# Performance work log

Hardware: AMD Instinct MI355X
Metric: run time of the kernel (lower is better)

The kernel has to match this reference:

```python
import jax, jax.numpy as jnp
import numpy as np

PATCH = 3
ALPHA = 0.5
EPS = 1e-12  # F.normalize default eps


def _unfold(x, p):
    # nn.Unfold(kernel_size=p, padding=p//2) then reshape(B, C, p*p, H*W)
    B, C, H, W = x.shape
    pad = p // 2
    xp = jnp.pad(x, ((0, 0), (0, 0), (pad, pad), (pad, pad)))
    # kernel positions row-major, matching torch unfold channel-major layout
    pats = jnp.stack([xp[:, :, i:i + H, j:j + W]
                      for i in range(p) for j in range(p)], axis=2)  # [B,C,K,H,W]
    return pats.reshape(B, C, p * p, H * W)


def setup_inputs() -> dict:
    key = jax.random.key(0)
    k1, k2 = jax.random.split(key)
    B, C, H, W = 4, 32, 256, 256
    fe_lv = jax.random.normal(k1, (B, C, H, W), dtype=jnp.float32)
    fused_features = jax.random.normal(k2, (B, C, H, W), dtype=jnp.float32)
    return {"fe_lv": fe_lv, "fused_features": fused_features}


def reference(fe_lv, fused_features):
    B, C, H, W = fe_lv.shape
    N = H * W
    patches = _unfold(fused_features, PATCH)          # [B,C,K,N]
    fe_flat = fe_lv.reshape(B, C, N)                  # [B,C,N]

    # cosine similarity over channel dim
    pn = patches / jnp.maximum(jnp.linalg.norm(patches, axis=1, keepdims=True), EPS)
    fn = fe_flat / jnp.maximum(jnp.linalg.norm(fe_flat, axis=1, keepdims=True), EPS)
    cosine_sim = jnp.einsum('bckn,bcn->bnk', pn, fn)  # [B,N,K]
    cosine_weights = jax.nn.softmax(cosine_sim, axis=-1)

    # euclidean distance over channel dim
    dist = jnp.sqrt(jnp.sum((patches - fe_flat[:, :, None, :]) ** 2, axis=1))  # [B,K,N]
    euclidean_weights = jax.nn.softmax(-dist.transpose(0, 2, 1), axis=-1)      # [B,N,K]

    weights = ALPHA * cosine_weights + (1.0 - ALPHA) * euclidean_weights
    refined = jnp.einsum('bnk,bckn->bcn', weights, patches)  # [B,C,N]
    return refined.reshape(B, C, H, W) + fe_lv
```

## Files before the change

### kernel.cpp

```cpp
#include <hip/hip_runtime.h>
#include <math.h>

#define B_ 4
#define C_ 32
#define H_ 256
#define W_ 256
#define HW_ (H_ * W_)
#define K_ 9
#define TX 32
#define TY 4
#define HX 34
#define HY 6
#define HCH (HX * HY)
#define NOCT 4
#define FUH8 (NOCT * HCH)
#define EPS_ 1e-12f

typedef _Float16 h2v __attribute__((ext_vector_type(2)));
typedef _Float16 h8v __attribute__((ext_vector_type(8)));

#if defined(__has_builtin)
#if __has_builtin(__builtin_amdgcn_fdot2)
#define HAVE_FDOT2 1
#endif
#if __has_builtin(__builtin_amdgcn_cvt_pkrtz)
#define HAVE_PKRTZ 1
#endif
#endif

static __device__ __forceinline__ h2v pk2(float a, float b) {
#if defined(HAVE_PKRTZ)
    return __builtin_bit_cast(h2v, __builtin_amdgcn_cvt_pkrtz(a, b));
#else
    h2v r = {(_Float16)a, (_Float16)b};
    return r;
#endif
}

static __device__ __forceinline__ float dot2(h2v a, h2v b, float c) {
#if defined(HAVE_FDOT2)
    return __builtin_amdgcn_fdot2(a, b, c, false);
#else
    return c + (float)a[0] * (float)b[0] + (float)a[1] * (float)b[1];
#endif
}

__global__ __launch_bounds__(256, 6) void asfr_kernel(const float* __restrict__ fe,
                                                      const float* __restrict__ fu,
                                                      float* __restrict__ out) {
    __shared__ h8v lds8[FUH8];
    const int t = threadIdx.x;
    const int bx = blockIdx.x & 7;
    const int by = (blockIdx.x >> 3) & 63;
    const int b  = blockIdx.x >> 9;
    const int w0 = bx * TX, h0 = by * TY;

    const int x = t & 31;
    const int half = (t >> 5) & 1;
    const int y = t >> 6;
    const int c0 = half << 4;
    const int pxoff = b * (C_ * HW_) + (h0 + y) * W_ + (w0 + x);

    float fv[16];
#pragma unroll
    for (int cc = 0; cc < 16; ++cc) fv[cc] = fe[pxoff + (c0 + cc) * HW_];

    const float* fub = fu + b * (C_ * HW_);
#pragma unroll
    for (int j = 0; j < 3; ++j) {
        int u = t + j * 256;
        int oct = u / HCH;
        int pos = u - oct * HCH;
        int r = pos / HX;
        int col = pos - r * HX;
        int hh = h0 - 1 + r;
        int ww = w0 - 1 + col;
        bool ok = ((unsigned)hh < (unsigned)H_) && ((unsigned)ww < (unsigned)W_);
        int hcl = hh < 0 ? 0 : (hh > H_ - 1 ? H_ - 1 : hh);
        int wcl = ww < 0 ? 0 : (ww > W_ - 1 ? W_ - 1 : ww);
        const float* gp = fub + (oct * 8) * HW_ + hcl * W_ + wcl;
        float v[8];
#pragma unroll
        for (int c = 0; c < 8; ++c) v[c] = gp[c * HW_];
        float m = ok ? 1.f : 0.f;
#pragma unroll
        for (int c = 0; c < 8; ++c) v[c] *= m;
        h8v hv;
#pragma unroll
        for (int c = 0; c < 4; ++c) {
            h2v p = pk2(v[2 * c], v[2 * c + 1]);
            hv[2 * c] = p[0];
            hv[2 * c + 1] = p[1];
        }
        lds8[u] = hv;
    }
    if (t < FUH8 - 768) {
        int u = t + 768;
        int oct = u / HCH;
        int pos = u - oct * HCH;
        int r = pos / HX;
        int col = pos - r * HX;
        int hh = h0 - 1 + r;
        int ww = w0 - 1 + col;
        bool ok = ((unsigned)hh < (unsigned)H_) && ((unsigned)ww < (unsigned)W_);
        int hcl = hh < 0 ? 0 : (hh > H_ - 1 ? H_ - 1 : hh);
        int wcl = ww < 0 ? 0 : (ww > W_ - 1 ? W_ - 1 : ww);
        const float* gp = fub + (oct * 8) * HW_ + hcl * W_ + wcl;
        float v[8];
#pragma unroll
        for (int c = 0; c < 8; ++c) v[c] = gp[c * HW_];
        float m = ok ? 1.f : 0.f;
#pragma unroll
        for (int c = 0; c < 8; ++c) v[c] *= m;
        h8v hv;
#pragma unroll
        for (int c = 0; c < 4; ++c) {
            h2v p = pk2(v[2 * c], v[2 * c + 1]);
            hv[2 * c] = p[0];
            hv[2 * c + 1] = p[1];
        }
        lds8[u] = hv;
    }

    h8v fe8[2];
#pragma unroll
    for (int j = 0; j < 2; ++j) {
#pragma unroll
        for (int c = 0; c < 4; ++c) {
            h2v p = pk2(fv[8 * j + 2 * c], fv[8 * j + 2 * c + 1]);
            fe8[j][2 * c] = p[0];
            fe8[j][2 * c + 1] = p[1];
        }
    }
    __syncthreads();

    const int hc = (y + 1) * HX + (x + 1);
    const int koff[K_] = {-HX - 1, -HX, -HX + 1, -1, 0, 1, HX - 1, HX, HX + 1};

    float dot[K_], psq[K_];
#pragma unroll
    for (int k = 0; k < K_; ++k) { dot[k] = 0.f; psq[k] = 0.f; }
    float fsq = 0.f;

#pragma unroll
    for (int j = 0; j < 2; ++j) {
        const int oct = 2 * half + j;
        h8v fq = fe8[j];
        h2v fA0 = __builtin_shufflevector(fq, fq, 0, 1);
        h2v fA1 = __builtin_shufflevector(fq, fq, 2, 3);
        h2v fA2 = __builtin_shufflevector(fq, fq, 4, 5);
        h2v fA3 = __builtin_shufflevector(fq, fq, 6, 7);
        fsq = dot2(fA0, fA0, fsq);
        fsq = dot2(fA1, fA1, fsq);
        fsq = dot2(fA2, fA2, fsq);
        fsq = dot2(fA3, fA3, fsq);
        const h8v* fubase = &lds8[oct * HCH + hc];
#pragma unroll
        for (int k = 0; k < K_; ++k) {
            h8v p8 = fubase[koff[k]];
            h2v p0 = __builtin_shufflevector(p8, p8, 0, 1);
            h2v p1 = __builtin_shufflevector(p8, p8, 2, 3);
            h2v p2 = __builtin_shufflevector(p8, p8, 4, 5);
            h2v p3 = __builtin_shufflevector(p8, p8, 6, 7);
            dot[k] = dot2(p0, fA0, dot[k]);
            dot[k] = dot2(p1, fA1, dot[k]);
            dot[k] = dot2(p2, fA2, dot[k]);
            dot[k] = dot2(p3, fA3, dot[k]);
            psq[k] = dot2(p0, p0, psq[k]);
            psq[k] = dot2(p1, p1, psq[k]);
            psq[k] = dot2(p2, p2, psq[k]);
            psq[k] = dot2(p3, p3, psq[k]);
        }
    }

#pragma unroll
    for (int k = 0; k < K_; ++k) {
        dot[k] += __shfl_xor(dot[k], 32);
        psq[k] += __shfl_xor(psq[k], 32);
    }
    fsq += __shfl_xor(fsq, 32);

    float nf = fmaxf(sqrtf(fsq), EPS_);
    float cosv[K_], negd[K_];
#pragma unroll
    for (int k = 0; k < K_; ++k) {
        float np = fmaxf(sqrtf(psq[k]), EPS_);
        cosv[k] = __fdividef(dot[k], np * nf);
        float dsq = fmaxf(psq[k] - 2.f * dot[k] + fsq, 0.f);
        negd[k] = -sqrtf(dsq);
    }

    float m1 = cosv[0], m2 = negd[0];
#pragma unroll
    for (int k = 1; k < K_; ++k) { m1 = fmaxf(m1, cosv[k]); m2 = fmaxf(m2, negd[k]); }
    float s1 = 0.f, s2 = 0.f, e1[K_], e2[K_];
#pragma unroll
    for (int k = 0; k < K_; ++k) {
        e1[k] = __expf(cosv[k] - m1);
        e2[k] = __expf(negd[k] - m2);
        s1 += e1[k]; s2 += e2[k];
    }
    float r1 = __fdividef(0.5f, s1), r2 = __fdividef(0.5f, s2);
    h2v w2[K_];
#pragma unroll
    for (int k = 0; k < K_; ++k) {
        float wk = fmaf(e1[k], r1, e2[k] * r2);
        _Float16 wh = (_Float16)wk;
        h2v tmp = {wh, wh};
        w2[k] = tmp;
    }

#pragma unroll
    for (int j = 0; j < 2; ++j) {
        const int oct = 2 * half + j;
        const h8v* fubase = &lds8[oct * HCH + hc];
        h2v a0 = {(_Float16)0, (_Float16)0};
        h2v a1 = a0, a2 = a0, a3 = a0;
#pragma unroll
        for (int k = 0; k < K_; ++k) {
            h8v p8 = fubase[koff[k]];
            a0 += w2[k] * __builtin_shufflevector(p8, p8, 0, 1);
            a1 += w2[k] * __builtin_shufflevector(p8, p8, 2, 3);
            a2 += w2[k] * __builtin_shufflevector(p8, p8, 4, 5);
            a3 += w2[k] * __builtin_shufflevector(p8, p8, 6, 7);
        }
        h8v fq = fe8[j];
        const int cg = oct * 8;
        out[pxoff + (cg + 0) * HW_] = (float)(fq[0] + a0[0]);
        out[pxoff + (cg + 1) * HW_] = (float)(fq[1] + a0[1]);
        out[pxoff + (cg + 2) * HW_] = (float)(fq[2] + a1[0]);
        out[pxoff + (cg + 3) * HW_] = (float)(fq[3] + a1[1]);
        out[pxoff + (cg + 4) * HW_] = (float)(fq[4] + a2[0]);
        out[pxoff + (cg + 5) * HW_] = (float)(fq[5] + a2[1]);
        out[pxoff + (cg + 6) * HW_] = (float)(fq[6] + a3[0]);
        out[pxoff + (cg + 7) * HW_] = (float)(fq[7] + a3[1]);
    }
}

extern "C" void kernel_launch(void* const* d_in, const int* in_sizes, int n_in,
                              void* d_out, int out_size, void* d_ws, size_t ws_size,
                              hipStream_t stream) {
    const float* fe = (const float*)d_in[0];
    const float* fu = (const float*)d_in[1];
    float* out = (float*)d_out;
    dim3 grid((W_ / TX) * (H_ / TY) * B_), block(256);
    hipLaunchKernelGGL(asfr_kernel, grid, block, 0, stream, fe, fu, out);
}
```

Before: 33.28 us.

## Process two batches per block with double-buffered LDS and prefetched second tile

Each block now handles the same spatial tile for two batch images, b0 and b0+2, and the grid is halved. The second batch's halo tile is loaded into registers while the first batch is computed, then written to a second LDS buffer, so global latency overlaps with compute. Halo address and mask computation is hoisted and shared by both batches, and the LDS layout is padded to 256 entries per octet so index math uses shifts. In exchange the kernel holds 32 extra prefetch registers and twice the LDS, which may reduce occupancy, and the grid has fewer blocks.

New measurement: 34.09 us. +2.4%, slower.

```diff
diff --git a/kernel.cpp b/kernel.cpp
--- a/kernel.cpp
+++ b/kernel.cpp
@@ -13,7 +13,6 @@
 #define HY 6
 #define HCH (HX * HY)
 #define NOCT 4
-#define FUH8 (NOCT * HCH)
 #define EPS_ 1e-12f
 
 typedef _Float16 h2v __attribute__((ext_vector_type(2)));
@@ -48,29 +47,29 @@
 __global__ __launch_bounds__(256, 6) void asfr_kernel(const float* __restrict__ fe,
                                                       const float* __restrict__ fu,
                                                       float* __restrict__ out) {
-    __shared__ h8v lds8[FUH8];
+    __shared__ h8v lds8[2][NOCT * 256];
     const int t = threadIdx.x;
     const int bx = blockIdx.x & 7;
     const int by = (blockIdx.x >> 3) & 63;
-    const int b  = blockIdx.x >> 9;
+    const int b0 = blockIdx.x >> 9;
     const int w0 = bx * TX, h0 = by * TY;
+    const int TILE2 = 2 * C_ * HW_;
 
     const int x = t & 31;
     const int half = (t >> 5) & 1;
     const int y = t >> 6;
     const int c0 = half << 4;
-    const int pxoff = b * (C_ * HW_) + (h0 + y) * W_ + (w0 + x);
-
-    float fv[16];
-#pragma unroll
-    for (int cc = 0; cc < 16; ++cc) fv[cc] = fe[pxoff + (c0 + cc) * HW_];
-
-    const float* fub = fu + b * (C_ * HW_);
-#pragma unroll
-    for (int j = 0; j < 3; ++j) {
+    const int pxoff0 = b0 * (C_ * HW_) + (h0 + y) * W_ + (w0 + x);
+
+    int goff[4];
+    float msk[4];
+    bool vld[4];
+#pragma unroll
+    for (int j = 0; j < 4; ++j) {
         int u = t + j * 256;
-        int oct = u / HCH;
-        int pos = u - oct * HCH;
+        int oct = u >> 8;
+        int pos = u & 255;
+        vld[j] = pos < HCH;
         int r = pos / HX;
         int col = pos - r * HX;
         int hh = h0 - 1 + r;
@@ -78,162 +77,275 @@
         bool ok = ((unsigned)hh < (unsigned)H_) && ((unsigned)ww < (unsigned)W_);
         int hcl = hh < 0 ? 0 : (hh > H_ - 1 ? H_ - 1 : hh);
         int wcl = ww < 0 ? 0 : (ww > W_ - 1 ? W_ - 1 : ww);
-        const float* gp = fub + (oct * 8) * HW_ + hcl * W_ + wcl;
-        float v[8];
-#pragma unroll
-        for (int c = 0; c < 8; ++c) v[c] = gp[c * HW_];
-        float m = ok ? 1.f : 0.f;
-#pragma unroll
-        for (int c = 0; c < 8; ++c) v[c] *= m;
-        h8v hv;
-#pragma unroll
-        for (int c = 0; c < 4; ++c) {
-            h2v p = pk2(v[2 * c], v[2 * c + 1]);
-            hv[2 * c] = p[0];
-            hv[2 * c + 1] = p[1];
-        }
-        lds8[u] = hv;
-    }
-    if (t < FUH8 - 768) {
-        int u = t + 768;
-        int oct = u / HCH;
-        int pos = u - oct * HCH;
-        int r = pos / HX;
-        int col = pos - r * HX;
-        int hh = h0 - 1 + r;
-        int ww = w0 - 1 + col;
-        bool ok = ((unsigned)hh < (unsigned)H_) && ((unsigned)ww < (unsigned)W_);
-        int hcl = hh < 0 ? 0 : (hh > H_ - 1 ? H_ - 1 : hh);
-        int wcl = ww < 0 ? 0 : (ww > W_ - 1 ? W_ - 1 : ww);
-        const float* gp = fub + (oct * 8) * HW_ + hcl * W_ + wcl;
-        float v[8];
-#pragma unroll
-        for (int c = 0; c < 8; ++c) v[c] = gp[c * HW_];
-        float m = ok ? 1.f : 0.f;
-#pragma unroll
-        for (int c = 0; c < 8; ++c) v[c] *= m;
-        h8v hv;
-#pragma unroll
-        for (int c = 0; c < 4; ++c) {
-            h2v p = pk2(v[2 * c], v[2 * c + 1]);
-            hv[2 * c] = p[0];
-            hv[2 * c + 1] = p[1];
-        }
-        lds8[u] = hv;
-    }
-
-    h8v fe8[2];
-#pragma unroll
-    for (int j = 0; j < 2; ++j) {
+        goff[j] = (oct * 8) * HW_ + hcl * W_ + wcl;
+        msk[j] = ok ? 1.f : 0.f;
+    }
+
+    const float* fub0 = fu + b0 * (C_ * HW_);
+
+    float fv[16];
+#pragma unroll
+    for (int cc = 0; cc < 16; ++cc) fv[cc] = fe[pxoff0 + (c0 + cc) * HW_];
+
+#pragma unroll
+    for (int j = 0; j < 4; ++j) {
+        if (vld[j]) {
+            float v[8];
+#pragma unroll
+            for (int c = 0; c < 8; ++c) v[c] = fub0[goff[j] + c * HW_] * msk[j];
+            h8v hv;
+#pragma unroll
+            for (int c = 0; c < 4; ++c) {
+                h2v p = pk2(v[2 * c], v[2 * c + 1]);
+                hv[2 * c] = p[0];
+                hv[2 * c + 1] = p[1];
+            }
+            lds8[0][t + j * 256] = hv;
+        }
+    }
+    h8v fe80[2];
+#pragma unroll
+    for (int j = 0; j < 2; ++j)
 #pragma unroll
         for (int c = 0; c < 4; ++c) {
             h2v p = pk2(fv[8 * j + 2 * c], fv[8 * j + 2 * c + 1]);
-            fe8[j][2 * c] = p[0];
-            fe8[j][2 * c + 1] = p[1];
-        }
-    }
+            fe80[j][2 * c] = p[0];
+            fe80[j][2 * c + 1] = p[1];
+        }
     __syncthreads();
+
+    float s1[32];
+#pragma unroll
+    for (int j = 0; j < 4; ++j) {
+        if (vld[j]) {
+#pragma unroll
+            for (int c = 0; c < 8; ++c) s1[8 * j + c] = fub0[TILE2 + goff[j] + c * HW_];
+        }
+    }
 
     const int hc = (y + 1) * HX + (x + 1);
     const int koff[K_] = {-HX - 1, -HX, -HX + 1, -1, 0, 1, HX - 1, HX, HX + 1};
 
-    float dot[K_], psq[K_];
-#pragma unroll
-    for (int k = 0; k < K_; ++k) { dot[k] = 0.f; psq[k] = 0.f; }
-    float fsq = 0.f;
-
-#pragma unroll
-    for (int j = 0; j < 2; ++j) {
-        const int oct = 2 * half + j;
-        h8v fq = fe8[j];
-        h2v fA0 = __builtin_shufflevector(fq, fq, 0, 1);
-        h2v fA1 = __builtin_shufflevector(fq, fq, 2, 3);
-        h2v fA2 = __builtin_shufflevector(fq, fq, 4, 5);
-        h2v fA3 = __builtin_shufflevector(fq, fq, 6, 7);
-        fsq = dot2(fA0, fA0, fsq);
-        fsq = dot2(fA1, fA1, fsq);
-        fsq = dot2(fA2, fA2, fsq);
-        fsq = dot2(fA3, fA3, fsq);
-        const h8v* fubase = &lds8[oct * HCH + hc];
-#pragma unroll
-        for (int k = 0; k < K_; ++k) {
-            h8v p8 = fubase[koff[k]];
-            h2v p0 = __builtin_shufflevector(p8, p8, 0, 1);
-            h2v p1 = __builtin_shufflevector(p8, p8, 2, 3);
-            h2v p2 = __builtin_shufflevector(p8, p8, 4, 5);
-            h2v p3 = __builtin_shufflevector(p8, p8, 6, 7);
-            dot[k] = dot2(p0, fA0, dot[k]);
-            dot[k] = dot2(p1, fA1, dot[k]);
-            dot[k] = dot2(p2, fA2, dot[k]);
-            dot[k] = dot2(p3, fA3, dot[k]);
-            psq[k] = dot2(p0, p0, psq[k]);
-            psq[k] = dot2(p1, p1, psq[k]);
-            psq[k] = dot2(p2, p2, psq[k]);
-            psq[k] = dot2(p3, p3, psq[k]);
-        }
-    }
-
-#pragma unroll
-    for (int k = 0; k < K_; ++k) {
-        dot[k] += __shfl_xor(dot[k], 32);
-        psq[k] += __shfl_xor(psq[k], 32);
-    }
-    fsq += __shfl_xor(fsq, 32);
-
-    float nf = fmaxf(sqrtf(fsq), EPS_);
-    float cosv[K_], negd[K_];
-#pragma unroll
-    for (int k = 0; k < K_; ++k) {
-        float np = fmaxf(sqrtf(psq[k]), EPS_);
-        cosv[k] = __fdividef(dot[k], np * nf);
-        float dsq = fmaxf(psq[k] - 2.f * dot[k] + fsq, 0.f);
-        negd[k] = -sqrtf(dsq);
-    }
-
-    float m1 = cosv[0], m2 = negd[0];
-#pragma unroll
-    for (int k = 1; k < K_; ++k) { m1 = fmaxf(m1, cosv[k]); m2 = fmaxf(m2, negd[k]); }
-    float s1 = 0.f, s2 = 0.f, e1[K_], e2[K_];
-#pragma unroll
-    for (int k = 0; k < K_; ++k) {
-        e1[k] = __expf(cosv[k] - m1);
-        e2[k] = __expf(negd[k] - m2);
-        s1 += e1[k]; s2 += e2[k];
-    }
-    float r1 = __fdividef(0.5f, s1), r2 = __fdividef(0.5f, s2);
-    h2v w2[K_];
-#pragma unroll
-    for (int k = 0; k < K_; ++k) {
-        float wk = fmaf(e1[k], r1, e2[k] * r2);
-        _Float16 wh = (_Float16)wk;
-        h2v tmp = {wh, wh};
-        w2[k] = tmp;
-    }
-
-#pragma unroll
-    for (int j = 0; j < 2; ++j) {
-        const int oct = 2 * half + j;
-        const h8v* fubase = &lds8[oct * HCH + hc];
-        h2v a0 = {(_Float16)0, (_Float16)0};
-        h2v a1 = a0, a2 = a0, a3 = a0;
-#pragma unroll
-        for (int k = 0; k < K_; ++k) {
-            h8v p8 = fubase[koff[k]];
-            a0 += w2[k] * __builtin_shufflevector(p8, p8, 0, 1);
-            a1 += w2[k] * __builtin_shufflevector(p8, p8, 2, 3);
-            a2 += w2[k] * __builtin_shufflevector(p8, p8, 4, 5);
-            a3 += w2[k] * __builtin_shufflevector(p8, p8, 6, 7);
-        }
-        h8v fq = fe8[j];
-        const int cg = oct * 8;
-        out[pxoff + (cg + 0) * HW_] = (float)(fq[0] + a0[0]);
-        out[pxoff + (cg + 1) * HW_] = (float)(fq[1] + a0[1]);
-        out[pxoff + (cg + 2) * HW_] = (float)(fq[2] + a1[0]);
-        out[pxoff + (cg + 3) * HW_] = (float)(fq[3] + a1[1]);
-        out[pxoff + (cg + 4) * HW_] = (float)(fq[4] + a2[0]);
-        out[pxoff + (cg + 5) * HW_] = (float)(fq[5] + a2[1]);
-        out[pxoff + (cg + 6) * HW_] = (float)(fq[6] + a3[0]);
-        out[pxoff + (cg + 7) * HW_] = (float)(fq[7] + a3[1]);
+    {
+        float dot[K_], psq[K_];
+#pragma unroll
+        for (int k = 0; k < K_; ++k) { dot[k] = 0.f; psq[k] = 0.f; }
+        float fsq = 0.f;
+#pragma unroll
+        for (int j = 0; j < 2; ++j) {
+            const int oct = 2 * half + j;
+            h8v fq = fe80[j];
+            h2v fA0 = __builtin_shufflevector(fq, fq, 0, 1);
+            h2v fA1 = __builtin_shufflevector(fq, fq, 2, 3);
+            h2v fA2 = __builtin_shufflevector(fq, fq, 4, 5);
+            h2v fA3 = __builtin_shufflevector(fq, fq, 6, 7);
+            fsq = dot2(fA0, fA0, fsq);
+            fsq = dot2(fA1, fA1, fsq);
+            fsq = dot2(fA2, fA2, fsq);
+            fsq = dot2(fA3, fA3, fsq);
+            const h8v* fubase = &lds8[0][(oct << 8) + hc];
+#pragma unroll
+            for (int k = 0; k < K_; ++k) {
+                h8v p8 = fubase[koff[k]];
+                h2v p0 = __builtin_shufflevector(p8, p8, 0, 1);
+                h2v p1 = __builtin_shufflevector(p8, p8, 2, 3);
+                h2v p2 = __builtin_shufflevector(p8, p8, 4, 5);
+                h2v p3 = __builtin_shufflevector(p8, p8, 6, 7);
+                dot[k] = dot2(p0, fA0, dot[k]);
+                dot[k] = dot2(p1, fA1, dot[k]);
+                dot[k] = dot2(p2, fA2, dot[k]);
+                dot[k] = dot2(p3, fA3, dot[k]);
+                psq[k] = dot2(p0, p0, psq[k]);
+                psq[k] = dot2(p1, p1, psq[k]);
+                psq[k] = dot2(p2, p2, psq[k]);
+                psq[k] = dot2(p3, p3, psq[k]);
+            }
+        }
+#pragma unroll
+        for (int k = 0; k < K_; ++k) {
+            dot[k] += __shfl_xor(dot[k], 32);
+            psq[k] += __shfl_xor(psq[k], 32);
+        }
+        fsq += __shfl_xor(fsq, 32);
+
+        float nf = fmaxf(sqrtf(fsq), EPS_);
+        float cosv[K_], negd[K_];
+#pragma unroll
+        for (int k = 0; k < K_; ++k) {
+            float np = fmaxf(sqrtf(psq[k]), EPS_);
+            cosv[k] = __fdividef(dot[k], np * nf);
+            float dsq = fmaxf(psq[k] - 2.f * dot[k] + fsq, 0.f);
+            negd[k] = -sqrtf(dsq);
+        }
+        float m1 = cosv[0], m2 = negd[0];
+#pragma unroll
+        for (int k = 1; k < K_; ++k) { m1 = fmaxf(m1, cosv[k]); m2 = fmaxf(m2, negd[k]); }
+        float s1x = 0.f, s2x = 0.f, e1[K_], e2[K_];
+#pragma unroll
+        for (int k = 0; k < K_; ++k) {
+            e1[k] = __expf(cosv[k] - m1);
+            e2[k] = __expf(negd[k] - m2);
+            s1x += e1[k]; s2x += e2[k];
+        }
+        float r1 = __fdividef(0.5f, s1x), r2 = __fdividef(0.5f, s2x);
+        h2v w2[K_];
+#pragma unroll
+        for (int k = 0; k < K_; ++k) {
+            float wk = fmaf(e1[k], r1, e2[k] * r2);
+            _Float16 wh = (_Float16)wk;
+            h2v tmp = {wh, wh};
+            w2[k] = tmp;
+        }
+#pragma unroll
+        for (int j = 0; j < 2; ++j) {
+            const int oct = 2 * half + j;
+            const h8v* fubase = &lds8[0][(oct << 8) + hc];
+            h2v a0 = {(_Float16)0, (_Float16)0};
+            h2v a1 = a0, a2 = a0, a3 = a0;
+#pragma unroll
+            for (int k = 0; k < K_; ++k) {
+                h8v p8 = fubase[koff[k]];
+                a0 += w2[k] * __builtin_shufflevector(p8, p8, 0, 1);
+                a1 += w2[k] * __builtin_shufflevector(p8, p8, 2, 3);
+                a2 += w2[k] * __builtin_shufflevector(p8, p8, 4, 5);
+                a3 += w2[k] * __builtin_shufflevector(p8, p8, 6, 7);
+            }
+            h8v fq = fe80[j];
+            const int cg = oct * 8;
+            out[pxoff0 + (cg + 0) * HW_] = (float)(fq[0] + a0[0]);
+            out[pxoff0 + (cg + 1) * HW_] = (float)(fq[1] + a0[1]);
+            out[pxoff0 + (cg + 2) * HW_] = (float)(fq[2] + a1[0]);
+            out[pxoff0 + (cg + 3) * HW_] = (float)(fq[3] + a1[1]);
+            out[pxoff0 + (cg + 4) * HW_] = (float)(fq[4] + a2[0]);
+            out[pxoff0 + (cg + 5) * HW_] = (float)(fq[5] + a2[1]);
+            out[pxoff0 + (cg + 6) * HW_] = (float)(fq[6] + a3[0]);
+            out[pxoff0 + (cg + 7) * HW_] = (float)(fq[7] + a3[1]);
+        }
+    }
+
+#pragma unroll
+    for (int j = 0; j < 4; ++j) {
+        if (vld[j]) {
+            h8v hv;
+#pragma unroll
+            for (int c = 0; c < 4; ++c) {
+                h2v p = pk2(s1[8 * j + 2 * c] * msk[j], s1[8 * j + 2 * c + 1] * msk[j]);
+                hv[2 * c] = p[0];
+                hv[2 * c + 1] = p[1];
+            }
+            lds8[1][t + j * 256] = hv;
+        }
+    }
+    __syncthreads();
+
+    const int pxoff1 = pxoff0 + TILE2;
+    float fv1[16];
+#pragma unroll
+    for (int cc = 0; cc < 16; ++cc) fv1[cc] = fe[pxoff1 + (c0 + cc) * HW_];
+    h8v fe81[2];
+#pragma unroll
+    for (int j = 0; j < 2; ++j)
+#pragma unroll
+        for (int c = 0; c < 4; ++c) {
+            h2v p = pk2(fv1[8 * j + 2 * c], fv1[8 * j + 2 * c + 1]);
+            fe81[j][2 * c] = p[0];
+            fe81[j][2 * c + 1] = p[1];
+        }
+    {
+        float dot[K_], psq[K_];
+#pragma unroll
+        for (int k = 0; k < K_; ++k) { dot[k] = 0.f; psq[k] = 0.f; }
+        float fsq = 0.f;
+#pragma unroll
+        for (int j = 0; j < 2; ++j) {
+            const int oct = 2 * half + j;
+            h8v fq = fe81[j];
+            h2v fA0 = __builtin_shufflevector(fq, fq, 0, 1);
+            h2v fA1 = __builtin_shufflevector(fq, fq, 2, 3);
+            h2v fA2 = __builtin_shufflevector(fq, fq, 4, 5);
+            h2v fA3 = __builtin_shufflevector(fq, fq, 6, 7);
+            fsq = dot2(fA0, fA0, fsq);
+            fsq = dot2(fA1, fA1, fsq);
+            fsq = dot2(fA2, fA2, fsq);
+            fsq = dot2(fA3, fA3, fsq);
+            const h8v* fubase = &lds8[1][(oct << 8) + hc];
+#pragma unroll
+            for (int k = 0; k < K_; ++k) {
+                h8v p8 = fubase[koff[k]];
+                h2v p0 = __builtin_shufflevector(p8, p8, 0, 1);
+                h2v p1 = __builtin_shufflevector(p8, p8, 2, 3);
+                h2v p2 = __builtin_shufflevector(p8, p8, 4, 5);
+                h2v p3 = __builtin_shufflevector(p8, p8, 6, 7);
+                dot[k] = dot2(p0, fA0, dot[k]);
+                dot[k] = dot2(p1, fA1, dot[k]);
+                dot[k] = dot2(p2, fA2, dot[k]);
+                dot[k] = dot2(p3, fA3, dot[k]);
+                psq[k] = dot2(p0, p0, psq[k]);
+                psq[k] = dot2(p1, p1, psq[k]);
+                psq[k] = dot2(p2, p2, psq[k]);
+                psq[k] = dot2(p3, p3, psq[k]);
+            }
+        }
+#pragma unroll
+        for (int k = 0; k < K_; ++k) {
+            dot[k] += __shfl_xor(dot[k], 32);
+            psq[k] += __shfl_xor(psq[k], 32);
+        }
+        fsq += __shfl_xor(fsq, 32);
+
+        float nf = fmaxf(sqrtf(fsq), EPS_);
+        float cosv[K_], negd[K_];
+#pragma unroll
+        for (int k = 0; k < K_; ++k) {
+            float np = fmaxf(sqrtf(psq[k]), EPS_);
+            cosv[k] = __fdividef(dot[k], np * nf);
+            float dsq = fmaxf(psq[k] - 2.f * dot[k] + fsq, 0.f);
+            negd[k] = -sqrtf(dsq);
+        }
+        float m1 = cosv[0], m2 = negd[0];
+#pragma unroll
+        for (int k = 1; k < K_; ++k) { m1 = fmaxf(m1, cosv[k]); m2 = fmaxf(m2, negd[k]); }
+        float s1x = 0.f, s2x = 0.f, e1[K_], e2[K_];
+#pragma unroll
+        for (int k = 0; k < K_; ++k) {
+            e1[k] = __expf(cosv[k] - m1);
+            e2[k] = __expf(negd[k] - m2);
+            s1x += e1[k]; s2x += e2[k];
+        }
+        float r1 = __fdividef(0.5f, s1x), r2 = __fdividef(0.5f, s2x);
+        h2v w2[K_];
+#pragma unroll
+        for (int k = 0; k < K_; ++k) {
+            float wk = fmaf(e1[k], r1, e2[k] * r2);
+            _Float16 wh = (_Float16)wk;
+            h2v tmp = {wh, wh};
+            w2[k] = tmp;
+        }
+#pragma unroll
+        for (int j = 0; j < 2; ++j) {
+            const int oct = 2 * half + j;
+            const h8v* fubase = &lds8[1][(oct << 8) + hc];
+            h2v a0 = {(_Float16)0, (_Float16)0};
+            h2v a1 = a0, a2 = a0, a3 = a0;
+#pragma unroll
+            for (int k = 0; k < K_; ++k) {
+                h8v p8 = fubase[koff[k]];
+                a0 += w2[k] * __builtin_shufflevector(p8, p8, 0, 1);
+                a1 += w2[k] * __builtin_shufflevector(p8, p8, 2, 3);
+                a2 += w2[k] * __builtin_shufflevector(p8, p8, 4, 5);
+                a3 += w2[k] * __builtin_shufflevector(p8, p8, 6, 7);
+            }
+            h8v fq = fe81[j];
+            const int cg = oct * 8;
+            out[pxoff1 + (cg + 0) * HW_] = (float)(fq[0] + a0[0]);
+            out[pxoff1 + (cg + 1) * HW_] = (float)(fq[1] + a0[1]);
+            out[pxoff1 + (cg + 2) * HW_] = (float)(fq[2] + a1[0]);
+            out[pxoff1 + (cg + 3) * HW_] = (float)(fq[3] + a1[1]);
+            out[pxoff1 + (cg + 4) * HW_] = (float)(fq[4] + a2[0]);
+            out[pxoff1 + (cg + 5) * HW_] = (float)(fq[5] + a2[1]);
+            out[pxoff1 + (cg + 6) * HW_] = (float)(fq[6] + a3[0]);
+            out[pxoff1 + (cg + 7) * HW_] = (float)(fq[7] + a3[1]);
+        }
     }
 }
 
@@ -243,6 +355,6 @@
     const float* fe = (const float*)d_in[0];
     const float* fu = (const float*)d_in[1];
     float* out = (float*)d_out;
-    dim3 grid((W_ / TX) * (H_ / TY) * B_), block(256);
+    dim3 grid(8 * 64 * 2), block(256);
     hipLaunchKernelGGL(asfr_kernel, grid, block, 0, stream, fe, fu, out);
 }
```

## Reshape tile to 64x2 and batch all global loads before LDS staging

Applied to the files above, without the earlier changes.

Changes the spatial tile from 32x4 to 64x2 pixels per block, so the halo row width becomes 66 and each wavefront covers 32 contiguous columns with both channel halves. It also precomputes all gather offsets and masks, then issues every global load (fe and halo units) up front before packing to fp16 and writing LDS, raising memory-level parallelism. The halo grows from 816 to 1056 units per block, meaning more redundant loads and LDS (about 16.9 KB), and more registers held for the 40 in-flight floats, which may cut occupancy.

Result: slower. 37.19 us (+11.8%).

```diff
diff --git a/kernel.cpp b/kernel.cpp
--- a/kernel.cpp
+++ b/kernel.cpp
@@ -7,13 +7,13 @@
 #define W_ 256
 #define HW_ (H_ * W_)
 #define K_ 9
-#define TX 32
-#define TY 4
-#define HX 34
-#define HY 6
+#define TX 64
+#define TY 2
+#define HX 66
+#define HY 4
 #define HCH (HX * HY)
 #define NOCT 4
-#define FUH8 (NOCT * HCH)
+#define NUNITS (NOCT * HCH)
 #define EPS_ 1e-12f
 
 typedef _Float16 h2v __attribute__((ext_vector_type(2)));
@@ -48,26 +48,26 @@
 __global__ __launch_bounds__(256, 6) void asfr_kernel(const float* __restrict__ fe,
                                                       const float* __restrict__ fu,
                                                       float* __restrict__ out) {
-    __shared__ h8v lds8[FUH8];
+    __shared__ h8v lds8[NUNITS];
     const int t = threadIdx.x;
-    const int bx = blockIdx.x & 7;
-    const int by = (blockIdx.x >> 3) & 63;
+    const int bx = blockIdx.x & 3;
+    const int by = (blockIdx.x >> 2) & 127;
     const int b  = blockIdx.x >> 9;
     const int w0 = bx * TX, h0 = by * TY;
 
-    const int x = t & 31;
-    const int half = (t >> 5) & 1;
-    const int y = t >> 6;
+    const int l = t & 63;
+    const int wv = t >> 6;
+    const int half = l >> 5;
+    const int px = (l & 31) + 32 * wv;
+    const int x = px & 63;
+    const int y = px >> 6;
     const int c0 = half << 4;
     const int pxoff = b * (C_ * HW_) + (h0 + y) * W_ + (w0 + x);
 
-    float fv[16];
-#pragma unroll
-    for (int cc = 0; cc < 16; ++cc) fv[cc] = fe[pxoff + (c0 + cc) * HW_];
-
-    const float* fub = fu + b * (C_ * HW_);
-#pragma unroll
-    for (int j = 0; j < 3; ++j) {
+    int goff[4];
+    float msk[4];
+#pragma unroll
+    for (int j = 0; j < 4; ++j) {
         int u = t + j * 256;
         int oct = u / HCH;
         int pos = u - oct * HCH;
@@ -78,24 +78,13 @@
         bool ok = ((unsigned)hh < (unsigned)H_) && ((unsigned)ww < (unsigned)W_);
         int hcl = hh < 0 ? 0 : (hh > H_ - 1 ? H_ - 1 : hh);
         int wcl = ww < 0 ? 0 : (ww > W_ - 1 ? W_ - 1 : ww);
-        const float* gp = fub + (oct * 8) * HW_ + hcl * W_ + wcl;
-        float v[8];
-#pragma unroll
-        for (int c = 0; c < 8; ++c) v[c] = gp[c * HW_];
-        float m = ok ? 1.f : 0.f;
-#pragma unroll
-        for (int c = 0; c < 8; ++c) v[c] *= m;
-        h8v hv;
-#pragma unroll
-        for (int c = 0; c < 4; ++c) {
-            h2v p = pk2(v[2 * c], v[2 * c + 1]);
-            hv[2 * c] = p[0];
-            hv[2 * c + 1] = p[1];
-        }
-        lds8[u] = hv;
-    }
-    if (t < FUH8 - 768) {
-        int u = t + 768;
+        goff[j] = (oct * 8) * HW_ + hcl * W_ + wcl;
+        msk[j] = ok ? 1.f : 0.f;
+    }
+    int goffT = 0;
+    float mskT = 0.f;
+    if (t < NUNITS - 1024) {
+        int u = t + 1024;
         int oct = u / HCH;
         int pos = u - oct * HCH;
         int r = pos / HX;
@@ -105,32 +94,54 @@
         bool ok = ((unsigned)hh < (unsigned)H_) && ((unsigned)ww < (unsigned)W_);
         int hcl = hh < 0 ? 0 : (hh > H_ - 1 ? H_ - 1 : hh);
         int wcl = ww < 0 ? 0 : (ww > W_ - 1 ? W_ - 1 : ww);
-        const float* gp = fub + (oct * 8) * HW_ + hcl * W_ + wcl;
-        float v[8];
-#pragma unroll
-        for (int c = 0; c < 8; ++c) v[c] = gp[c * HW_];
-        float m = ok ? 1.f : 0.f;
-#pragma unroll
-        for (int c = 0; c < 8; ++c) v[c] *= m;
-        h8v hv;
-#pragma unroll
-        for (int c = 0; c < 4; ++c) {
-            h2v p = pk2(v[2 * c], v[2 * c + 1]);
-            hv[2 * c] = p[0];
-            hv[2 * c + 1] = p[1];
-        }
-        lds8[u] = hv;
-    }
-
+        goffT = (oct * 8) * HW_ + hcl * W_ + wcl;
+        mskT = ok ? 1.f : 0.f;
+    }
+
+    float fv[16];
+#pragma unroll
+    for (int cc = 0; cc < 16; ++cc) fv[cc] = fe[pxoff + (c0 + cc) * HW_];
     h8v fe8[2];
 #pragma unroll
-    for (int j = 0; j < 2; ++j) {
+    for (int j = 0; j < 2; ++j)
 #pragma unroll
         for (int c = 0; c < 4; ++c) {
             h2v p = pk2(fv[8 * j + 2 * c], fv[8 * j + 2 * c + 1]);
             fe8[j][2 * c] = p[0];
             fe8[j][2 * c + 1] = p[1];
         }
+
+    const float* fub = fu + b * (C_ * HW_);
+    float s[32];
+#pragma unroll
+    for (int j = 0; j < 4; ++j)
+#pragma unroll
+        for (int c = 0; c < 8; ++c) s[8 * j + c] = fub[goff[j] + c * HW_];
+    float sT[8];
+    if (t < NUNITS - 1024) {
+#pragma unroll
+        for (int c = 0; c < 8; ++c) sT[c] = fub[goffT + c * HW_];
+    }
+#pragma unroll
+    for (int j = 0; j < 4; ++j) {
+        h8v hv;
+#pragma unroll
+        for (int c = 0; c < 4; ++c) {
+            h2v p = pk2(s[8 * j + 2 * c] * msk[j], s[8 * j + 2 * c + 1] * msk[j]);
+            hv[2 * c] = p[0];
+            hv[2 * c + 1] = p[1];
+        }
+        lds8[t + j * 256] = hv;
+    }
+    if (t < NUNITS - 1024) {
+        h8v hv;
+#pragma unroll
+        for (int c = 0; c < 4; ++c) {
+            h2v p = pk2(sT[2 * c] * mskT, sT[2 * c + 1] * mskT);
+            hv[2 * c] = p[0];
+            hv[2 * c + 1] = p[1];
+        }
+        lds8[t + 1024] = hv;
     }
     __syncthreads();
 
```
